# Performance work log

Hardware: AMD Instinct MI355X
Metric: run time of the kernel (lower is better)

The kernel has to match this reference:

```python
import jax, jax.numpy as jnp
import numpy as np
from jax import lax

B, H, W = 2, 240, 1216
ITER, NUM = 3, 9
CH = ITER * NUM  # 27


def setup_inputs() -> dict:
    key = jax.random.key(0)
    ks = jax.random.split(key, 6)
    inp = jax.random.normal(ks[0], (B, 1, H, W), dtype=jnp.float32)
    guide = jax.random.normal(ks[1], (B, CH, H, W), dtype=jnp.float32)
    sp_dep = jax.random.uniform(ks[2], (B, 1, H, W), dtype=jnp.float32)
    confidence = jax.random.normal(ks[3], (B, 1, H, W), dtype=jnp.float32)
    conv_w = jax.random.normal(ks[4], (3 * CH, CH, 3, 3), dtype=jnp.float32) * 0.05
    conv_b = jax.random.normal(ks[5], (3 * CH,), dtype=jnp.float32) * 0.05
    # fixed 3x3 tap offsets, rows are (dx, dy) -- matches mode='xy'
    tap = jnp.array([[-1, -1], [0, -1], [1, -1], [-1, 0], [0, 0], [1, 0], [-1, 1], [0, 1], [1, 1]], dtype=jnp.float32)
    return {"input": inp, "guide": guide, "sp_dep": sp_dep, "confidence": confidence,
            "conv_w": conv_w, "conv_b": conv_b, "tap": tap}


def _bilinear_zeros(img, px, py):
    """img: [B,H,W]; px,py: [B,N,H,W] pixel coords. Matches F.grid_sample
    (bilinear, padding_mode='zeros', align_corners=False): the normalized grid
    built in get_refgrid maps exactly to pixel coord = x + tap + offset."""
    Hh, Ww = img.shape[-2], img.shape[-1]
    x0f = jnp.floor(px)
    y0f = jnp.floor(py)
    wx1 = px - x0f
    wy1 = py - y0f
    x0 = x0f.astype(jnp.int32)
    y0 = y0f.astype(jnp.int32)
    flat = img.reshape(img.shape[0], Hh * Ww)

    def gather(xi, yi):
        valid = (xi >= 0) & (xi < Ww) & (yi >= 0) & (yi < Hh)
        idx = jnp.clip(yi, 0, Hh - 1) * Ww + jnp.clip(xi, 0, Ww - 1)
        v = jax.vmap(lambda f, i: f[i])(flat, idx)  # [B,N,H,W]
        return jnp.where(valid, v, jnp.zeros((), img.dtype))

    v00 = gather(x0, y0)
    v01 = gather(x0 + 1, y0)
    v10 = gather(x0, y0 + 1)
    v11 = gather(x0 + 1, y0 + 1)
    return ((1 - wy1) * ((1 - wx1) * v00 + wx1 * v01)
            + wy1 * ((1 - wx1) * v10 + wx1 * v11))


def reference(input, guide, sp_dep, confidence, conv_w, conv_b, tap):
    Bb, _, Hh, Ww = input.shape
    out = lax.conv_general_dilated(
        guide, conv_w, window_strides=(1, 1), padding=((1, 1), (1, 1)),
        dimension_numbers=("NCHW", "OIHW", "NCHW")) + conv_b[None, :, None, None]
    # split into offsets (2*ch) and affinities (ch)
    offset = out[:, :2 * CH].reshape(Bb, ITER, NUM, 2, Hh, Ww)  # b iter n (x,y) h w
    aff = out[:, 2 * CH:].reshape(Bb, ITER, NUM, Hh, Ww)
    aff = jax.nn.softmax(aff, axis=2)  # softmax over the NUM taps

    conf = jax.nn.sigmoid(confidence[:, 0]) * jnp.sign(sp_dep[:, 0])  # [B,H,W]
    spd = sp_dep[:, 0]

    xg = jnp.arange(Ww, dtype=jnp.float32)
    yg = jnp.arange(Hh, dtype=jnp.float32)
    # sampling pixel coords: x + tap_x + offset_x  (exact grid_sample equivalence)
    px = offset[:, :, :, 0] + tap[None, None, :, 0, None, None] + xg[None, None, None, None, :]
    py = offset[:, :, :, 1] + tap[None, None, :, 1, None, None] + yg[None, None, None, :, None]

    cur = input[:, 0]  # [B,H,W]
    feat_init = cur
    inter = []
    for i in range(ITER):
        vals = _bilinear_zeros(cur, px[:, i], py[:, i])  # [B,NUM,H,W]
        agg = jnp.sum(vals * aff[:, i], axis=1)          # affinity-weighted sum
        cur = (1 - conf) * agg + conf * spd
        inter.append(cur)
    pred = cur[:, None]
    return pred, feat_init[:, None], jnp.stack(inter, axis=0)[:, :, None]
```

## Files before the change

### kernel.cpp

```cpp
#include <hip/hip_runtime.h>
#include <math.h>

#define B_ 2
#define H_ 240
#define W_ 1216
#define CH_ 27
#define NUM_ 9
#define PIX_ (B_ * H_ * W_)
#define CHP 32
#define CHL 40
#define TX 32
#define TY 8
#define HALO_W (TX + 2)
#define HALO_H (TY + 2)

typedef __attribute__((ext_vector_type(8))) __bf16 bf16x8;
typedef __attribute__((ext_vector_type(16))) float f32x16;

__global__ __launch_bounds__(256) void transpose_guide(
    const float* __restrict__ guide, __bf16* __restrict__ gt)
{
    int pix = blockIdx.x * 256 + threadIdx.x;
    if (pix >= PIX_) return;
    int b = pix / (H_ * W_);
    int off = pix - b * (H_ * W_);
    __align__(16) __bf16 tmp[CHP];
    const float* src = guide + (size_t)b * CH_ * H_ * W_ + off;
    #pragma unroll
    for (int ic = 0; ic < CH_; ++ic)
        tmp[ic] = (__bf16)src[(size_t)ic * (H_ * W_)];
    #pragma unroll
    for (int ic = CH_; ic < CHP; ++ic) tmp[ic] = (__bf16)0.f;
    bf16x8* dst = (bf16x8*)(gt + (size_t)pix * CHP);
    const bf16x8* s8 = (const bf16x8*)tmp;
    #pragma unroll
    for (int c = 0; c < 4; ++c) dst[c] = s8[c];
}

__global__ __launch_bounds__(256) void prep_weights(
    const float* __restrict__ conv_w, __bf16* __restrict__ wlin)
{
    int idx = blockIdx.x * 256 + threadIdx.x;
    if (idx >= 3 * 9 * 2 * 64) return;
    int lane = idx & 63;
    int grp = idx >> 6;
    int ks = grp & 1;
    int tapi = (grp >> 1) % 9;
    int it = (grp >> 1) / 9;
    int n = lane & 31;
    int half = lane >> 5;
    __align__(16) __bf16 v8[8];
    #pragma unroll
    for (int j = 0; j < 8; ++j) {
        int ic = ks * 16 + half * 8 + j;
        float v = 0.f;
        if (ic < CH_ && n < CH_) {
            int oc = (n < 18) ? (it * 18 + n) : (54 + it * NUM_ + (n - 18));
            v = conv_w[(size_t)(oc * CH_ + ic) * 9 + tapi];
        }
        v8[j] = (__bf16)v;
    }
    *(bf16x8*)(wlin + (size_t)idx * 8) = *(const bf16x8*)v8;
}

__global__ __launch_bounds__(256, 2) void dyspn_iter_mfma(
    const __bf16* __restrict__ gt, const __bf16* __restrict__ wlin,
    const float* __restrict__ conv_b, const float* __restrict__ tap,
    const float* __restrict__ confidence, const float* __restrict__ sp_dep,
    const float* __restrict__ cur_in, float* __restrict__ out_cur,
    float* __restrict__ pred, float* __restrict__ feat,
    const float* __restrict__ input, int iter)
{
    __shared__ __align__(16) char smem[256 * 33 * 4];
    __bf16* sG = (__bf16*)smem;
    float*  sC = (float*)smem;
    __shared__ float sBias[CH_ + 1];

    const int tid = threadIdx.x;
    const int lane = tid & 63;
    const int w = tid >> 6;
    const int xl = lane & 31;
    const int half = lane >> 5;
    const int tileX0 = blockIdx.x * TX;
    const int tileY0 = blockIdx.y * TY;
    const int b = blockIdx.z;

    if (tid < CH_) {
        int n = tid;
        int oc = (n < 18) ? (iter * 18 + n) : (54 + iter * NUM_ + (n - 18));
        sBias[tid] = conv_b[oc];
    }

    for (int idx = tid; idx < HALO_H * HALO_W * 4; idx += 256) {
        int chunk = idx & 3;
        int p = idx >> 2;
        int row = p / HALO_W;
        int px = p - row * HALO_W;
        int gy = tileY0 + row - 1;
        int gx = tileX0 + px - 1;
        uint4 v = make_uint4(0, 0, 0, 0);
        if (gx >= 0 && gx < W_ && gy >= 0 && gy < H_) {
            size_t pg = (size_t)b * (H_ * W_) + (size_t)gy * W_ + gx;
            v = ((const uint4*)(gt + pg * CHP))[chunk];
        }
        *(uint4*)((char*)sG + ((size_t)(row * HALO_W + px) * CHL + chunk * 8) * 2) = v;
    }

    bf16x8 Bf[18];
    {
        const __bf16* wb = wlin + ((size_t)iter * 18 * 64 + lane) * 8;
        #pragma unroll
        for (int i = 0; i < 18; ++i)
            Bf[i] = *(const bf16x8*)(wb + (size_t)i * 64 * 8);
    }

    f32x16 acc0 = {0,0,0,0,0,0,0,0,0,0,0,0,0,0,0,0};
    f32x16 acc1 = {0,0,0,0,0,0,0,0,0,0,0,0,0,0,0,0};

    __syncthreads();

    #pragma unroll
    for (int kw = 0; kw < 3; ++kw) {
        #pragma unroll
        for (int ks = 0; ks < 2; ++ks) {
            bf16x8 A4[4];
            #pragma unroll
            for (int d = 0; d < 4; ++d) {
                const __bf16* ap = sG + (size_t)((2 * w + d) * HALO_W + xl + kw) * CHL
                                 + ks * 16 + half * 8;
                A4[d] = *(const bf16x8*)ap;
            }
            #pragma unroll
            for (int kh = 0; kh < 3; ++kh) {
                int t = kh * 3 + kw;
                acc0 = __builtin_amdgcn_mfma_f32_32x32x16_bf16(A4[kh],     Bf[t * 2 + ks], acc0, 0, 0, 0);
                acc1 = __builtin_amdgcn_mfma_f32_32x32x16_bf16(A4[kh + 1], Bf[t * 2 + ks], acc1, 0, 0, 0);
            }
        }
    }

    __syncthreads();

    {
        int ch = xl;
        #pragma unroll
        for (int a = 0; a < 2; ++a) {
            const f32x16 A = a ? acc1 : acc0;
            int ra = 2 * w + a;
            #pragma unroll
            for (int r = 0; r < 16; ++r) {
                int px_x = (r & 3) + 8 * (r >> 2) + 4 * half;
                sC[(ra * 32 + px_x) * 33 + ch] = A[r];
            }
        }
    }

    __syncthreads();

    const int x = tileX0 + (tid & 31);
    const int y = tileY0 + (tid >> 5);
    float v27[CH_];
    #pragma unroll
    for (int j = 0; j < CH_; ++j) v27[j] = sC[tid * 33 + j] + sBias[j];

    float m = v27[18];
    #pragma unroll
    for (int n = 1; n < 9; ++n) m = fmaxf(m, v27[18 + n]);
    float a[9]; float s = 0.f;
    #pragma unroll
    for (int n = 0; n < 9; ++n) { a[n] = __expf(v27[18 + n] - m); s += a[n]; }
    const float inv_s = 1.f / s;

    const float* cur = cur_in + (size_t)b * (H_ * W_);
    float agg = 0.f;
    #pragma unroll
    for (int n = 0; n < 9; ++n) {
        float px = v27[2 * n]     + tap[2 * n]     + (float)x;
        float py = v27[2 * n + 1] + tap[2 * n + 1] + (float)y;
        float x0f = floorf(px), y0f = floorf(py);
        float wx = px - x0f, wy = py - y0f;
        int x0 = (int)x0f, y0 = (int)y0f;
        bool vx0 = (x0 >= 0) && (x0 < W_);
        bool vx1 = (x0 + 1 >= 0) && (x0 + 1 < W_);
        bool vy0 = (y0 >= 0) && (y0 < H_);
        bool vy1 = (y0 + 1 >= 0) && (y0 + 1 < H_);
        int cx0 = min(max(x0, 0), W_ - 1), cx1 = min(max(x0 + 1, 0), W_ - 1);
        int cy0 = min(max(y0, 0), H_ - 1), cy1 = min(max(y0 + 1, 0), H_ - 1);
        float v00 = 0.f, v01 = 0.f, v10 = 0.f, v11 = 0.f;
        if (vy0) {
            const float* row = cur + (size_t)cy0 * W_;
            if (vx0) v00 = row[cx0];
            if (vx1) v01 = row[cx1];
        }
        if (vy1) {
            const float* row = cur + (size_t)cy1 * W_;
            if (vx0) v10 = row[cx0];
            if (vx1) v11 = row[cx1];
        }
        float val = (1.f - wy) * ((1.f - wx) * v00 + wx * v01)
                  +        wy  * ((1.f - wx) * v10 + wx * v11);
        agg = fmaf(val, a[n] * inv_s, agg);
    }

    const int pix = b * (H_ * W_) + y * W_ + x;
    float c  = confidence[pix];
    float sp = sp_dep[pix];
    float sgn = (sp > 0.f) ? 1.f : ((sp < 0.f) ? -1.f : 0.f);
    float conf = sgn / (1.f + __expf(-c));
    float nc = (1.f - conf) * agg + conf * sp;

    out_cur[pix] = nc;
    if (pred) pred[pix] = nc;
    if (feat) feat[pix] = input[pix];
}

__global__ __launch_bounds__(256) void dyspn_iter_fp32(
    const float* __restrict__ guide, const float* __restrict__ conv_w,
    const float* __restrict__ conv_b, const float* __restrict__ tap,
    const float* __restrict__ confidence, const float* __restrict__ sp_dep,
    const float* __restrict__ cur_in, float* __restrict__ out_cur,
    float* __restrict__ pred, float* __restrict__ feat,
    const float* __restrict__ input, int iter)
{
    __shared__ float sg[CH_ * HALO_H * HALO_W];
    const int tid = threadIdx.x;
    const int tileX0 = blockIdx.x * TX;
    const int tileY0 = blockIdx.y * TY;
    const int b = blockIdx.z;
    for (int idx = tid; idx < CH_ * HALO_H * HALO_W; idx += 256) {
        int ic  = idx / (HALO_H * HALO_W);
        int rem = idx % (HALO_H * HALO_W);
        int ly = rem / HALO_W;
        int lx = rem % HALO_W;
        int gy = tileY0 + ly - 1;
        int gx = tileX0 + lx - 1;
        float v = 0.f;
        if (gx >= 0 && gx < W_ && gy >= 0 && gy < H_)
            v = guide[((b * CH_ + ic) * H_ + gy) * W_ + gx];
        sg[idx] = v;
    }
    __syncthreads();
    const int tx = tid % TX;
    const int ty = tid / TX;
    const int x = tileX0 + tx;
    const int y = tileY0 + ty;
    const int oc0 = iter * 18;
    const int oc1 = 54 + iter * NUM_;
    float acc[27];
    #pragma unroll
    for (int j = 0; j < 18; ++j) acc[j] = conv_b[oc0 + j];
    #pragma unroll
    for (int j = 0; j < 9; ++j)  acc[18 + j] = conv_b[oc1 + j];
    for (int ic = 0; ic < CH_; ++ic) {
        float g[9];
        #pragma unroll
        for (int t = 0; t < 9; ++t) {
            int dy = t / 3, dx = t % 3;
            g[t] = sg[ic * (HALO_H * HALO_W) + (ty + dy) * HALO_W + (tx + dx)];
        }
        #pragma unroll
        for (int j = 0; j < 18; ++j) {
            const float* wp = conv_w + ((oc0 + j) * CH_ + ic) * 9;
            #pragma unroll
            for (int t = 0; t < 9; ++t) acc[j] = fmaf(wp[t], g[t], acc[j]);
        }
        #pragma unroll
        for (int j = 0; j < 9; ++j) {
            const float* wp = conv_w + ((oc1 + j) * CH_ + ic) * 9;
            #pragma unroll
            for (int t = 0; t < 9; ++t) acc[18 + j] = fmaf(wp[t], g[t], acc[18 + j]);
        }
    }
    float m = acc[18];
    #pragma unroll
    for (int n = 1; n < 9; ++n) m = fmaxf(m, acc[18 + n]);
    float a[9]; float s = 0.f;
    #pragma unroll
    for (int n = 0; n < 9; ++n) { a[n] = __expf(acc[18 + n] - m); s += a[n]; }
    const float inv_s = 1.f / s;
    const float* cur = cur_in + b * (H_ * W_);
    float agg = 0.f;
    #pragma unroll
    for (int n = 0; n < 9; ++n) {
        float px = acc[2 * n]     + tap[2 * n]     + (float)x;
        float py = acc[2 * n + 1] + tap[2 * n + 1] + (float)y;
        float x0f = floorf(px), y0f = floorf(py);
        float wx = px - x0f, wy = py - y0f;
        int x0 = (int)x0f, y0 = (int)y0f;
        bool vx0 = (x0 >= 0) && (x0 < W_);
        bool vx1 = (x0 + 1 >= 0) && (x0 + 1 < W_);
        bool vy0 = (y0 >= 0) && (y0 < H_);
        bool vy1 = (y0 + 1 >= 0) && (y0 + 1 < H_);
        int cx0 = min(max(x0, 0), W_ - 1), cx1 = min(max(x0 + 1, 0), W_ - 1);
        int cy0 = min(max(y0, 0), H_ - 1), cy1 = min(max(y0 + 1, 0), H_ - 1);
        float v00 = 0.f, v01 = 0.f, v10 = 0.f, v11 = 0.f;
        if (vy0) {
            const float* row = cur + cy0 * W_;
            if (vx0) v00 = row[cx0];
            if (vx1) v01 = row[cx1];
        }
        if (vy1) {
            const float* row = cur + cy1 * W_;
            if (vx0) v10 = row[cx0];
            if (vx1) v11 = row[cx1];
        }
        float val = (1.f - wy) * ((1.f - wx) * v00 + wx * v01)
                  +        wy  * ((1.f - wx) * v10 + wx * v11);
        agg = fmaf(val, a[n] * inv_s, agg);
    }
    const int pix = b * (H_ * W_) + y * W_ + x;
    float c  = confidence[pix];
    float sp = sp_dep[pix];
    float sgn = (sp > 0.f) ? 1.f : ((sp < 0.f) ? -1.f : 0.f);
    float conf = sgn / (1.f + __expf(-c));
    float nc = (1.f - conf) * agg + conf * sp;
    out_cur[pix] = nc;
    if (pred) pred[pix] = nc;
    if (feat) feat[pix] = input[pix];
}

extern "C" void kernel_launch(void* const* d_in, const int* in_sizes, int n_in,
                              void* d_out, int out_size, void* d_ws, size_t ws_size,
                              hipStream_t stream) {
    (void)in_sizes; (void)n_in; (void)out_size;
    const float* input      = (const float*)d_in[0];
    const float* guide      = (const float*)d_in[1];
    const float* sp_dep     = (const float*)d_in[2];
    const float* confidence = (const float*)d_in[3];
    const float* conv_w     = (const float*)d_in[4];
    const float* conv_b     = (const float*)d_in[5];
    const float* tap        = (const float*)d_in[6];

    float* out   = (float*)d_out;
    const int P  = PIX_;
    float* pred  = out;
    float* feat  = out + P;
    float* inter = out + 2 * P;

    dim3 grid(W_ / TX, H_ / TY, B_);
    dim3 block(256);

    const size_t gt_bytes   = (size_t)PIX_ * CHP * 2;
    const size_t wlin_bytes = (size_t)3 * 9 * 2 * 64 * 8 * 2;

    if (ws_size >= gt_bytes + wlin_bytes) {
        __bf16* gt   = (__bf16*)d_ws;
        __bf16* wlin = (__bf16*)((char*)d_ws + gt_bytes);

        transpose_guide<<<(PIX_ + 255) / 256, 256, 0, stream>>>(guide, gt);
        prep_weights<<<(3 * 9 * 2 * 64 + 255) / 256, 256, 0, stream>>>(conv_w, wlin);

        for (int i = 0; i < 3; ++i) {
            const float* cur = (i == 0) ? input : (inter + (i - 1) * P);
            dyspn_iter_mfma<<<grid, block, 0, stream>>>(
                gt, wlin, conv_b, tap, confidence, sp_dep,
                cur, inter + i * P,
                (i == 2) ? pred : nullptr,
                (i == 0) ? feat : nullptr,
                input, i);
        }
    } else {
        for (int i = 0; i < 3; ++i) {
            const float* cur = (i == 0) ? input : (inter + (i - 1) * P);
            dyspn_iter_fp32<<<grid, block, 0, stream>>>(
                guide, conv_w, conv_b, tap, confidence, sp_dep,
                cur, inter + i * P,
                (i == 2) ? pred : nullptr,
                (i == 0) ? feat : nullptr,
                input, i);
        }
    }
}
```

Before: 217.2 us.

## Compute all three iterations' conv params in one kernel, separate propagation kernels

Replaces the guide-transpose kernel plus three fused conv+propagate kernels with one conv kernel that loads the fp32 guide halo directly into shared memory as bf16. That kernel computes all 81 output channels across the three iterations and writes per-pixel offsets and normalized affinities to a workspace buffer. Three lightweight propagation kernels then read these params and do the bilinear sampling. This removes the transpose pass and the repeated guide tile loads, but adds a large intermediate params write and read of 3×PIX×28 floats, and the strided per-channel guide loads may coalesce less well.

```diff
diff --git a/kernel.cpp b/kernel.cpp
--- a/kernel.cpp
+++ b/kernel.cpp
@@ -7,35 +7,15 @@
 #define CH_ 27
 #define NUM_ 9
 #define PIX_ (B_ * H_ * W_)
-#define CHP 32
-#define CHL 40
 #define TX 32
 #define TY 8
 #define HALO_W (TX + 2)
 #define HALO_H (TY + 2)
+#define CHL 40
+#define PCH 28
 
 typedef __attribute__((ext_vector_type(8))) __bf16 bf16x8;
 typedef __attribute__((ext_vector_type(16))) float f32x16;
-
-__global__ __launch_bounds__(256) void transpose_guide(
-    const float* __restrict__ guide, __bf16* __restrict__ gt)
-{
-    int pix = blockIdx.x * 256 + threadIdx.x;
-    if (pix >= PIX_) return;
-    int b = pix / (H_ * W_);
-    int off = pix - b * (H_ * W_);
-    __align__(16) __bf16 tmp[CHP];
-    const float* src = guide + (size_t)b * CH_ * H_ * W_ + off;
-    #pragma unroll
-    for (int ic = 0; ic < CH_; ++ic)
-        tmp[ic] = (__bf16)src[(size_t)ic * (H_ * W_)];
-    #pragma unroll
-    for (int ic = CH_; ic < CHP; ++ic) tmp[ic] = (__bf16)0.f;
-    bf16x8* dst = (bf16x8*)(gt + (size_t)pix * CHP);
-    const bf16x8* s8 = (const bf16x8*)tmp;
-    #pragma unroll
-    for (int c = 0; c < 4; ++c) dst[c] = s8[c];
-}
 
 __global__ __launch_bounds__(256) void prep_weights(
     const float* __restrict__ conv_w, __bf16* __restrict__ wlin)
@@ -63,18 +43,15 @@
     *(bf16x8*)(wlin + (size_t)idx * 8) = *(const bf16x8*)v8;
 }
 
-__global__ __launch_bounds__(256, 2) void dyspn_iter_mfma(
-    const __bf16* __restrict__ gt, const __bf16* __restrict__ wlin,
+__global__ __launch_bounds__(256, 2) void dyspn_conv81(
+    const float* __restrict__ guide, const __bf16* __restrict__ wlin,
     const float* __restrict__ conv_b, const float* __restrict__ tap,
-    const float* __restrict__ confidence, const float* __restrict__ sp_dep,
-    const float* __restrict__ cur_in, float* __restrict__ out_cur,
-    float* __restrict__ pred, float* __restrict__ feat,
-    const float* __restrict__ input, int iter)
+    float* __restrict__ params)
 {
-    __shared__ __align__(16) char smem[256 * 33 * 4];
-    __bf16* sG = (__bf16*)smem;
-    float*  sC = (float*)smem;
-    __shared__ float sBias[CH_ + 1];
+    __shared__ __align__(16) __bf16 sG[HALO_H * HALO_W * CHL];
+    __shared__ __align__(16) float sC[256 * 33];
+    __shared__ float sBias[81];
+    __shared__ float sTap[18];
 
     const int tid = threadIdx.x;
     const int lane = tid & 63;
@@ -85,98 +62,133 @@
     const int tileY0 = blockIdx.y * TY;
     const int b = blockIdx.z;
 
-    if (tid < CH_) {
-        int n = tid;
-        int oc = (n < 18) ? (iter * 18 + n) : (54 + iter * NUM_ + (n - 18));
+    if (tid < 81) {
+        int it = tid / 27, n = tid - it * 27;
+        int oc = (n < 18) ? (it * 18 + n) : (54 + it * NUM_ + (n - 18));
         sBias[tid] = conv_b[oc];
     }
-
-    for (int idx = tid; idx < HALO_H * HALO_W * 4; idx += 256) {
-        int chunk = idx & 3;
-        int p = idx >> 2;
-        int row = p / HALO_W;
-        int px = p - row * HALO_W;
+    if (tid >= 128 && tid < 146) sTap[tid - 128] = tap[tid - 128];
+
+    const float* gb = guide + (size_t)b * CH_ * H_ * W_;
+    for (int idx = tid; idx < 32 * (HALO_H * HALO_W); idx += 256) {
+        int ic = idx / (HALO_H * HALO_W);
+        int rem = idx - ic * (HALO_H * HALO_W);
+        int row = rem / HALO_W;
+        int px = rem - row * HALO_W;
         int gy = tileY0 + row - 1;
         int gx = tileX0 + px - 1;
-        uint4 v = make_uint4(0, 0, 0, 0);
-        if (gx >= 0 && gx < W_ && gy >= 0 && gy < H_) {
-            size_t pg = (size_t)b * (H_ * W_) + (size_t)gy * W_ + gx;
-            v = ((const uint4*)(gt + pg * CHP))[chunk];
-        }
-        *(uint4*)((char*)sG + ((size_t)(row * HALO_W + px) * CHL + chunk * 8) * 2) = v;
-    }
-
-    bf16x8 Bf[18];
-    {
-        const __bf16* wb = wlin + ((size_t)iter * 18 * 64 + lane) * 8;
-        #pragma unroll
-        for (int i = 0; i < 18; ++i)
-            Bf[i] = *(const bf16x8*)(wb + (size_t)i * 64 * 8);
-    }
-
-    f32x16 acc0 = {0,0,0,0,0,0,0,0,0,0,0,0,0,0,0,0};
-    f32x16 acc1 = {0,0,0,0,0,0,0,0,0,0,0,0,0,0,0,0};
-
-    __syncthreads();
-
-    #pragma unroll
-    for (int kw = 0; kw < 3; ++kw) {
-        #pragma unroll
-        for (int ks = 0; ks < 2; ++ks) {
-            bf16x8 A4[4];
-            #pragma unroll
-            for (int d = 0; d < 4; ++d) {
-                const __bf16* ap = sG + (size_t)((2 * w + d) * HALO_W + xl + kw) * CHL
-                                 + ks * 16 + half * 8;
-                A4[d] = *(const bf16x8*)ap;
-            }
-            #pragma unroll
-            for (int kh = 0; kh < 3; ++kh) {
-                int t = kh * 3 + kw;
-                acc0 = __builtin_amdgcn_mfma_f32_32x32x16_bf16(A4[kh],     Bf[t * 2 + ks], acc0, 0, 0, 0);
-                acc1 = __builtin_amdgcn_mfma_f32_32x32x16_bf16(A4[kh + 1], Bf[t * 2 + ks], acc1, 0, 0, 0);
-            }
-        }
-    }
-
-    __syncthreads();
-
-    {
-        int ch = xl;
-        #pragma unroll
-        for (int a = 0; a < 2; ++a) {
-            const f32x16 A = a ? acc1 : acc0;
-            int ra = 2 * w + a;
-            #pragma unroll
-            for (int r = 0; r < 16; ++r) {
-                int px_x = (r & 3) + 8 * (r >> 2) + 4 * half;
-                sC[(ra * 32 + px_x) * 33 + ch] = A[r];
-            }
-        }
-    }
-
+        float v = 0.f;
+        if (ic < CH_ && gx >= 0 && gx < W_ && gy >= 0 && gy < H_)
+            v = gb[(size_t)ic * (H_ * W_) + (size_t)gy * W_ + gx];
+        sG[rem * CHL + ic] = (__bf16)v;
+    }
     __syncthreads();
 
     const int x = tileX0 + (tid & 31);
     const int y = tileY0 + (tid >> 5);
-    float v27[CH_];
-    #pragma unroll
-    for (int j = 0; j < CH_; ++j) v27[j] = sC[tid * 33 + j] + sBias[j];
-
-    float m = v27[18];
-    #pragma unroll
-    for (int n = 1; n < 9; ++n) m = fmaxf(m, v27[18 + n]);
-    float a[9]; float s = 0.f;
-    #pragma unroll
-    for (int n = 0; n < 9; ++n) { a[n] = __expf(v27[18 + n] - m); s += a[n]; }
-    const float inv_s = 1.f / s;
+    const size_t pix = (size_t)b * (H_ * W_) + (size_t)y * W_ + x;
+
+    #pragma unroll 1
+    for (int it = 0; it < 3; ++it) {
+        bf16x8 Bf[18];
+        {
+            const __bf16* wb = wlin + ((size_t)it * 18 * 64 + lane) * 8;
+            #pragma unroll
+            for (int i = 0; i < 18; ++i)
+                Bf[i] = *(const bf16x8*)(wb + (size_t)i * 64 * 8);
+        }
+
+        f32x16 acc0 = {0,0,0,0,0,0,0,0,0,0,0,0,0,0,0,0};
+        f32x16 acc1 = {0,0,0,0,0,0,0,0,0,0,0,0,0,0,0,0};
+
+        #pragma unroll
+        for (int kw = 0; kw < 3; ++kw) {
+            #pragma unroll
+            for (int ks = 0; ks < 2; ++ks) {
+                bf16x8 A4[4];
+                #pragma unroll
+                for (int d = 0; d < 4; ++d) {
+                    const __bf16* ap = sG + (size_t)((2 * w + d) * HALO_W + xl + kw) * CHL
+                                     + ks * 16 + half * 8;
+                    A4[d] = *(const bf16x8*)ap;
+                }
+                #pragma unroll
+                for (int kh = 0; kh < 3; ++kh) {
+                    int t = kh * 3 + kw;
+                    acc0 = __builtin_amdgcn_mfma_f32_32x32x16_bf16(A4[kh],     Bf[t * 2 + ks], acc0, 0, 0, 0);
+                    acc1 = __builtin_amdgcn_mfma_f32_32x32x16_bf16(A4[kh + 1], Bf[t * 2 + ks], acc1, 0, 0, 0);
+                }
+            }
+        }
+
+        {
+            int ch = xl;
+            #pragma unroll
+            for (int a2 = 0; a2 < 2; ++a2) {
+                const f32x16 A = a2 ? acc1 : acc0;
+                int ra = 2 * w + a2;
+                #pragma unroll
+                for (int r = 0; r < 16; ++r) {
+                    int px_x = (r & 3) + 8 * (r >> 2) + 4 * half;
+                    sC[(ra * 32 + px_x) * 33 + ch] = A[r];
+                }
+            }
+        }
+        __syncthreads();
+
+        float v27[CH_];
+        #pragma unroll
+        for (int j = 0; j < CH_; ++j) v27[j] = sC[tid * 33 + j] + sBias[it * 27 + j];
+
+        float m = v27[18];
+        #pragma unroll
+        for (int n = 1; n < 9; ++n) m = fmaxf(m, v27[18 + n]);
+        float a[9]; float s = 0.f;
+        #pragma unroll
+        for (int n = 0; n < 9; ++n) { a[n] = __expf(v27[18 + n] - m); s += a[n]; }
+        const float inv_s = 1.f / s;
+
+        __align__(16) float o28[PCH];
+        #pragma unroll
+        for (int n = 0; n < 9; ++n) {
+            o28[2 * n]     = v27[2 * n]     + sTap[2 * n];
+            o28[2 * n + 1] = v27[2 * n + 1] + sTap[2 * n + 1];
+            o28[18 + n]    = a[n] * inv_s;
+        }
+        o28[27] = 0.f;
+
+        uint4* dst = (uint4*)(params + ((size_t)it * PIX_ + pix) * PCH);
+        const uint4* s4 = (const uint4*)o28;
+        #pragma unroll
+        for (int c = 0; c < 7; ++c) dst[c] = s4[c];
+
+        __syncthreads();
+    }
+}
+
+__global__ __launch_bounds__(256) void dyspn_prop(
+    const float* __restrict__ params, const float* __restrict__ confidence,
+    const float* __restrict__ sp_dep, const float* __restrict__ cur_in,
+    float* __restrict__ out_cur, float* __restrict__ pred, float* __restrict__ feat,
+    const float* __restrict__ input, int it)
+{
+    const int pix = blockIdx.x * 256 + threadIdx.x;
+    const int b = pix / (H_ * W_);
+    const int off = pix - b * (H_ * W_);
+    const int y = off / W_;
+    const int x = off - y * W_;
+
+    __align__(16) float o28[PCH];
+    const uint4* src = (const uint4*)(params + ((size_t)it * PIX_ + pix) * PCH);
+    #pragma unroll
+    for (int c = 0; c < 7; ++c) ((uint4*)o28)[c] = src[c];
 
     const float* cur = cur_in + (size_t)b * (H_ * W_);
     float agg = 0.f;
     #pragma unroll
     for (int n = 0; n < 9; ++n) {
-        float px = v27[2 * n]     + tap[2 * n]     + (float)x;
-        float py = v27[2 * n + 1] + tap[2 * n + 1] + (float)y;
+        float px = o28[2 * n]     + (float)x;
+        float py = o28[2 * n + 1] + (float)y;
         float x0f = floorf(px), y0f = floorf(py);
         float wx = px - x0f, wy = py - y0f;
         int x0 = (int)x0f, y0 = (int)y0f;
@@ -199,10 +211,9 @@
         }
         float val = (1.f - wy) * ((1.f - wx) * v00 + wx * v01)
                   +        wy  * ((1.f - wx) * v10 + wx * v11);
-        agg = fmaf(val, a[n] * inv_s, agg);
-    }
-
-    const int pix = b * (H_ * W_) + y * W_ + x;
+        agg = fmaf(val, o28[18 + n], agg);
+    }
+
     float c  = confidence[pix];
     float sp = sp_dep[pix];
     float sgn = (sp > 0.f) ? 1.f : ((sp < 0.f) ? -1.f : 0.f);
@@ -337,32 +348,31 @@
     float* feat  = out + P;
     float* inter = out + 2 * P;
 
-    dim3 grid(W_ / TX, H_ / TY, B_);
-    dim3 block(256);
-
-    const size_t gt_bytes   = (size_t)PIX_ * CHP * 2;
-    const size_t wlin_bytes = (size_t)3 * 9 * 2 * 64 * 8 * 2;
-
-    if (ws_size >= gt_bytes + wlin_bytes) {
-        __bf16* gt   = (__bf16*)d_ws;
-        __bf16* wlin = (__bf16*)((char*)d_ws + gt_bytes);
-
-        transpose_guide<<<(PIX_ + 255) / 256, 256, 0, stream>>>(guide, gt);
+    const size_t params_bytes = (size_t)3 * PIX_ * PCH * sizeof(float);
+    const size_t wlin_bytes   = (size_t)3 * 9 * 2 * 64 * 8 * 2;
+
+    if (ws_size >= params_bytes + wlin_bytes) {
+        float*  params = (float*)d_ws;
+        __bf16* wlin   = (__bf16*)((char*)d_ws + params_bytes);
+
         prep_weights<<<(3 * 9 * 2 * 64 + 255) / 256, 256, 0, stream>>>(conv_w, wlin);
+
+        dim3 cgrid(W_ / TX, H_ / TY, B_);
+        dyspn_conv81<<<cgrid, 256, 0, stream>>>(guide, wlin, conv_b, tap, params);
 
         for (int i = 0; i < 3; ++i) {
             const float* cur = (i == 0) ? input : (inter + (i - 1) * P);
-            dyspn_iter_mfma<<<grid, block, 0, stream>>>(
-                gt, wlin, conv_b, tap, confidence, sp_dep,
-                cur, inter + i * P,
+            dyspn_prop<<<PIX_ / 256, 256, 0, stream>>>(
+                params, confidence, sp_dep, cur, inter + i * P,
                 (i == 2) ? pred : nullptr,
                 (i == 0) ? feat : nullptr,
                 input, i);
         }
     } else {
+        dim3 grid(W_ / TX, H_ / TY, B_);
         for (int i = 0; i < 3; ++i) {
             const float* cur = (i == 0) ? input : (inter + (i - 1) * P);
-            dyspn_iter_fp32<<<grid, block, 0, stream>>>(
+            dyspn_iter_fp32<<<grid, 256, 0, stream>>>(
                 guide, conv_w, conv_b, tap, confidence, sp_dep,
                 cur, inter + i * P,
                 (i == 2) ? pred : nullptr,
```

New measurement: 367.2 us. +69.1%, slower.

## Swap MFMA operands and redistribute accumulators via lane shuffles instead of LDS

Applied to the files above, without the earlier changes.

The MFMA operands are swapped so each lane's accumulator holds channel values for a pixel rather than pixel values for a channel. A cross-half-wave shuffle then assembles all 27 channels per lane, which removes the LDS staging buffer, two barriers and the shared bias array. Weights are loaded in two batches of nine per k-slice instead of eighteen at once, and launch bounds are raised to four blocks per CU to allow higher occupancy. The cost is shuffle work and divergent selects on each lane, plus possible register spills under the tighter bound. The pixel-to-thread mapping changes, and lanes now read conv_b directly from global memory.

```diff
diff --git a/kernel.cpp b/kernel.cpp
--- a/kernel.cpp
+++ b/kernel.cpp
@@ -63,7 +63,7 @@
     *(bf16x8*)(wlin + (size_t)idx * 8) = *(const bf16x8*)v8;
 }
 
-__global__ __launch_bounds__(256, 2) void dyspn_iter_mfma(
+__global__ __launch_bounds__(256, 4) void dyspn_iter_v3(
     const __bf16* __restrict__ gt, const __bf16* __restrict__ wlin,
     const float* __restrict__ conv_b, const float* __restrict__ tap,
     const float* __restrict__ confidence, const float* __restrict__ sp_dep,
@@ -71,10 +71,7 @@
     float* __restrict__ pred, float* __restrict__ feat,
     const float* __restrict__ input, int iter)
 {
-    __shared__ __align__(16) char smem[256 * 33 * 4];
-    __bf16* sG = (__bf16*)smem;
-    float*  sC = (float*)smem;
-    __shared__ float sBias[CH_ + 1];
+    __shared__ __align__(16) __bf16 sG[HALO_H * HALO_W * CHL];
 
     const int tid = threadIdx.x;
     const int lane = tid & 63;
@@ -84,12 +81,6 @@
     const int tileX0 = blockIdx.x * TX;
     const int tileY0 = blockIdx.y * TY;
     const int b = blockIdx.z;
-
-    if (tid < CH_) {
-        int n = tid;
-        int oc = (n < 18) ? (iter * 18 + n) : (54 + iter * NUM_ + (n - 18));
-        sBias[tid] = conv_b[oc];
-    }
 
     for (int idx = tid; idx < HALO_H * HALO_W * 4; idx += 256) {
         int chunk = idx & 3;
@@ -103,26 +94,22 @@
             size_t pg = (size_t)b * (H_ * W_) + (size_t)gy * W_ + gx;
             v = ((const uint4*)(gt + pg * CHP))[chunk];
         }
-        *(uint4*)((char*)sG + ((size_t)(row * HALO_W + px) * CHL + chunk * 8) * 2) = v;
-    }
-
-    bf16x8 Bf[18];
-    {
-        const __bf16* wb = wlin + ((size_t)iter * 18 * 64 + lane) * 8;
-        #pragma unroll
-        for (int i = 0; i < 18; ++i)
-            Bf[i] = *(const bf16x8*)(wb + (size_t)i * 64 * 8);
-    }
+        *(uint4*)((char*)sG + ((size_t)(p * CHL) + chunk * 8) * 2) = v;
+    }
+    __syncthreads();
 
     f32x16 acc0 = {0,0,0,0,0,0,0,0,0,0,0,0,0,0,0,0};
     f32x16 acc1 = {0,0,0,0,0,0,0,0,0,0,0,0,0,0,0,0};
 
-    __syncthreads();
-
-    #pragma unroll
-    for (int kw = 0; kw < 3; ++kw) {
-        #pragma unroll
-        for (int ks = 0; ks < 2; ++ks) {
+    #pragma unroll
+    for (int ks = 0; ks < 2; ++ks) {
+        bf16x8 Bf9[9];
+        #pragma unroll
+        for (int t = 0; t < 9; ++t)
+            Bf9[t] = *(const bf16x8*)(wlin +
+                ((size_t)((iter * 9 + t) * 2 + ks) * 64 + lane) * 8);
+        #pragma unroll
+        for (int kw = 0; kw < 3; ++kw) {
             bf16x8 A4[4];
             #pragma unroll
             for (int d = 0; d < 4; ++d) {
@@ -133,35 +120,29 @@
             #pragma unroll
             for (int kh = 0; kh < 3; ++kh) {
                 int t = kh * 3 + kw;
-                acc0 = __builtin_amdgcn_mfma_f32_32x32x16_bf16(A4[kh],     Bf[t * 2 + ks], acc0, 0, 0, 0);
-                acc1 = __builtin_amdgcn_mfma_f32_32x32x16_bf16(A4[kh + 1], Bf[t * 2 + ks], acc1, 0, 0, 0);
+                acc0 = __builtin_amdgcn_mfma_f32_32x32x16_bf16(Bf9[t], A4[kh],     acc0, 0, 0, 0);
+                acc1 = __builtin_amdgcn_mfma_f32_32x32x16_bf16(Bf9[t], A4[kh + 1], acc1, 0, 0, 0);
             }
         }
     }
 
-    __syncthreads();
-
-    {
-        int ch = xl;
-        #pragma unroll
-        for (int a = 0; a < 2; ++a) {
-            const f32x16 A = a ? acc1 : acc0;
-            int ra = 2 * w + a;
-            #pragma unroll
-            for (int r = 0; r < 16; ++r) {
-                int px_x = (r & 3) + 8 * (r >> 2) + 4 * half;
-                sC[(ra * 32 + px_x) * 33 + ch] = A[r];
-            }
-        }
-    }
-
-    __syncthreads();
-
-    const int x = tileX0 + (tid & 31);
-    const int y = tileY0 + (tid >> 5);
+    float oth[16];
+    #pragma unroll
+    for (int r = 0; r < 16; ++r) {
+        float send = half ? acc0[r] : acc1[r];
+        oth[r] = __shfl_xor(send, 32, 64);
+    }
+
     float v27[CH_];
     #pragma unroll
-    for (int j = 0; j < CH_; ++j) v27[j] = sC[tid * 33 + j] + sBias[j];
+    for (int c = 0; c < CH_; ++c) {
+        int r = (c & 3) + 4 * (c >> 3);
+        int hc = (c >> 2) & 1;
+        float own = half ? acc1[r] : acc0[r];
+        float val = (hc == half) ? own : oth[r];
+        int oc = (c < 18) ? (iter * 18 + c) : (54 + iter * NUM_ + (c - 18));
+        v27[c] = val + conv_b[oc];
+    }
 
     float m = v27[18];
     #pragma unroll
@@ -171,6 +152,8 @@
     for (int n = 0; n < 9; ++n) { a[n] = __expf(v27[18 + n] - m); s += a[n]; }
     const float inv_s = 1.f / s;
 
+    const int x = tileX0 + xl;
+    const int y = tileY0 + 2 * w + half;
     const float* cur = cur_in + (size_t)b * (H_ * W_);
     float agg = 0.f;
     #pragma unroll
@@ -352,7 +335,7 @@
 
         for (int i = 0; i < 3; ++i) {
             const float* cur = (i == 0) ? input : (inter + (i - 1) * P);
-            dyspn_iter_mfma<<<grid, block, 0, stream>>>(
+            dyspn_iter_v3<<<grid, block, 0, stream>>>(
                 gt, wlin, conv_b, tap, confidence, sp_dep,
                 cur, inter + i * P,
                 (i == 2) ? pred : nullptr,
```

Measured after the change: 224.0 us. 3.1% more time.
